# Kernel tuning notes

Measured on AMD Instinct MI355X. Metric: run time of the kernel, lower is better.

The kernel has to match this reference:

```python
import jax, jax.numpy as jnp
import numpy as np

B, D_W, D_C, D_P = 4096, 2048, 1024, 2048
RANK = D_W // 4  # 512, per A_U/A_V shapes (d_w, d_w//4)


def setup_inputs() -> dict:
    key = jax.random.key(0)
    ks = jax.random.split(key, 10)
    return {
        "w_prev": jax.random.normal(ks[0], (B, D_W), jnp.float32),
        "z_t": jax.random.normal(ks[1], (B, D_P), jnp.float32),
        "c_t": jax.random.normal(ks[2], (B, D_C), jnp.float32),
        # params (mirroring flax init: A_diag zeros, A_U/A_V normal(0.01),
        # Dense kernels lecun_normal-ish scale, zero biases)
        "A_diag": jnp.zeros((D_W,), jnp.float32),
        "A_U": 0.01 * jax.random.normal(ks[3], (D_W, RANK), jnp.float32),
        "A_V": 0.01 * jax.random.normal(ks[4], (D_W, RANK), jnp.float32),
        "W_mod": jax.random.normal(ks[5], (D_C, D_W), jnp.float32) / np.sqrt(D_C),
        "b_mod": jnp.zeros((D_W,), jnp.float32),
        "W_B": jax.random.normal(ks[6], (D_C + D_P, D_W), jnp.float32) / np.sqrt(D_C + D_P),
        "b_B": jnp.zeros((D_W,), jnp.float32),
    }


def reference(w_prev, z_t, c_t, A_diag, A_U, A_V, W_mod, b_mod, W_B, b_B):
    # A = diag(tanh(A_diag)*0.9) + A_U @ A_V^T, row-scaled by modulation.
    # Equivalent (same math) without materializing [B, d_w, d_w]:
    #   (A * m[:, :, None]) @ w = m * (a_diag * w + A_U @ (A_V^T @ w))
    a_diag = jnp.tanh(A_diag) * 0.9                              # [d_w]
    modulation = jnp.tanh(c_t @ W_mod + b_mod)                   # [B, d_w]
    Aw = a_diag * w_prev + (w_prev @ A_V) @ A_U.T                # [B, d_w]
    Bt = jnp.concatenate([c_t, z_t], axis=-1) @ W_B + b_B        # [B, d_w]
    return modulation * Aw + Bt
```

## Files before the change

kernel.cpp:

```cpp
#include <hip/hip_runtime.h>


#define DEV __device__ __forceinline__

typedef __bf16 v8bf __attribute__((ext_vector_type(8)));
typedef __bf16 v4bf __attribute__((ext_vector_type(4)));
typedef float  v4f  __attribute__((ext_vector_type(4)));

typedef __attribute__((address_space(1))) const unsigned int* as1_cuint_ptr;
typedef __attribute__((address_space(3))) unsigned int*       as3_uint_ptr;

DEV void async16(const void* g, void* l) {
  __builtin_amdgcn_global_load_lds(
      (as1_cuint_ptr)(unsigned long long)g,
      (as3_uint_ptr)(unsigned long long)l,
      16, 0, 0);
}

DEV float tanh_fast(float x) {
  x = fminf(15.f, fmaxf(-15.f, x));
  float e = __expf(2.f * x);
  return (e - 1.f) / (e + 1.f);
}

__global__ void prep(const float* __restrict__ w, const float* __restrict__ z,
                     const float* __restrict__ c, const float* __restrict__ au,
                     const float* __restrict__ av,
                     const float* __restrict__ Wmod, const float* __restrict__ WB,
                     __bf16* __restrict__ wb, __bf16* __restrict__ zb,
                     __bf16* __restrict__ cb, __bf16* __restrict__ aub,
                     __bf16* __restrict__ avb,
                     __bf16* __restrict__ Wmodt, __bf16* __restrict__ WBt) {
  __shared__ float t[32][33];
  int b = blockIdx.x;
  if (b < 22528) {
    const float* src; __bf16* dst; int off;
    if (b < 8192)        { src = w;  dst = wb;  off = b; }
    else if (b < 16384)  { src = z;  dst = zb;  off = b - 8192; }
    else if (b < 20480)  { src = c;  dst = cb;  off = b - 16384; }
    else if (b < 21504)  { src = au; dst = aub; off = b - 20480; }
    else                 { src = av; dst = avb; off = b - 21504; }
    size_t i = (size_t)off * 1024 + (size_t)threadIdx.x * 4;
    float4 v = *reinterpret_cast<const float4*>(src + i);
    v4bf o;
    o.x = (__bf16)v.x; o.y = (__bf16)v.y; o.z = (__bf16)v.z; o.w = (__bf16)v.w;
    *reinterpret_cast<v4bf*>(dst + i) = o;
    return;
  }
  b -= 22528;
  const float* src; __bf16* dst; int R;
  if (b < 2048) { src = Wmod; dst = Wmodt; R = 1024; }
  else          { b -= 2048; src = WB; dst = WBt; R = 3072; }
  const int c0 = (b & 63) * 32, r0 = (b >> 6) * 32;
  const int C = 2048;
  const int tx = threadIdx.x & 31, ty = threadIdx.x >> 5;
#pragma unroll
  for (int rr = 0; rr < 32; rr += 8)
    t[ty + rr][tx] = src[(size_t)(r0 + ty + rr) * C + c0 + tx];
  __syncthreads();
#pragma unroll
  for (int rr = 0; rr < 32; rr += 8)
    dst[(size_t)(c0 + ty + rr) * R + r0 + tx] = (__bf16)t[tx][ty + rr];
}

__global__ __launch_bounds__(256, 2) void gemm_mt(
    const __bf16* __restrict__ A0, const __bf16* __restrict__ Bt,
    int N, int K, __bf16* __restrict__ out, const float* __restrict__ A_diag) {
  __shared__ __align__(16) __bf16 As[128 * 32];
  __shared__ __align__(16) __bf16 Bs[128 * 32];

  const int tid = threadIdx.x, lane = tid & 63, wid = tid >> 6;
  const int wm = wid >> 1, wn = wid & 1, l16 = lane & 15, quad = lane >> 4;
  const int m0 = blockIdx.y * 128, n0 = blockIdx.x * 128;
  const int sg_row = lane >> 2;
  const int sk = ((lane & 3) ^ ((lane >> 3) & 3)) * 8;
  const int qs = quad ^ ((l16 >> 1) & 3);

  v4f acc[4][4];
#pragma unroll
  for (int i = 0; i < 4; ++i)
#pragma unroll
    for (int j = 0; j < 4; ++j) { v4f zz = {0,0,0,0}; acc[i][j] = zz; }

  for (int k0 = 0; k0 < K; k0 += 32) {
    __syncthreads();
#pragma unroll
    for (int t = 0; t < 2; ++t) {
      const int chunk = wid * 2 + t;
      const int row = chunk * 16 + sg_row;
      async16((const void*)(A0 + (size_t)(m0 + row) * K + k0 + sk),
              (void*)&As[chunk * 512 + lane * 8]);
      async16((const void*)(Bt + (size_t)(n0 + row) * K + k0 + sk),
              (void*)&Bs[chunk * 512 + lane * 8]);
    }
    __syncthreads();
    const v8bf* Ap = reinterpret_cast<const v8bf*>(As);
    const v8bf* Bp = reinterpret_cast<const v8bf*>(Bs);
    v8bf a[4], b[4];
#pragma unroll
    for (int i = 0; i < 4; ++i) a[i] = Ap[(wm * 64 + i * 16 + l16) * 4 + qs];
#pragma unroll
    for (int j = 0; j < 4; ++j) b[j] = Bp[(wn * 64 + j * 16 + l16) * 4 + qs];
#pragma unroll
    for (int i = 0; i < 4; ++i)
#pragma unroll
      for (int j = 0; j < 4; ++j)
        acc[i][j] = __builtin_amdgcn_mfma_f32_16x16x32_bf16(a[i], b[j],
                                                            acc[i][j], 0, 0, 0);
  }

  const int mBase = m0 + wm * 64 + quad * 4;
  const int nBase = n0 + wn * 64 + l16;
#pragma unroll
  for (int j = 0; j < 4; ++j) {
    const int n = nBase + j * 16;
#pragma unroll
    for (int i = 0; i < 4; ++i)
#pragma unroll
      for (int r = 0; r < 4; ++r) {
        const int m = mBase + i * 16 + r;
        float v = acc[i][j][r];
        if (m == n) v += tanh_fast(A_diag[m]) * 0.9f;
        out[(size_t)m * N + n] = (__bf16)v;
      }
  }
}

__global__ __launch_bounds__(256, 2) void fused_main(
    const __bf16* __restrict__ c, const __bf16* __restrict__ z,
    const __bf16* __restrict__ w, const __bf16* __restrict__ Wmodt,
    const __bf16* __restrict__ Mt, const __bf16* __restrict__ WBt,
    const float* __restrict__ b_mod, const float* __restrict__ b_B,
    float* __restrict__ out) {
  constexpr int DC = 1024, DW = 2048, KB = 3072;
  __shared__ __align__(16) __bf16 As[128 * 128];
  __shared__ __align__(16) __bf16 Bs[128 * 128];

  const int tid = threadIdx.x, lane = tid & 63, wid = tid >> 6;
  const int wm = wid >> 1, wn = wid & 1, l16 = lane & 15, quad = lane >> 4;
  const int m0 = blockIdx.y * 128;
  const int n0 = blockIdx.x * 128;
  const int r4  = lane >> 4;
  const int s16 = lane & 15;

  v4f acc[4][4];
#pragma unroll
  for (int i = 0; i < 4; ++i)
#pragma unroll
    for (int j = 0; j < 4; ++j) { v4f zz = {0,0,0,0}; acc[i][j] = zz; }

  auto kstep = [&](const __bf16* gA, size_t lda, const __bf16* gB, size_t ldb,
                   int kA, int kB) {
    __syncthreads();
#pragma unroll
    for (int t = 0; t < 8; ++t) {
      const int row = wid * 32 + t * 4 + r4;
      const int gk = (s16 ^ (row & 15)) * 8;
      async16((const void*)(gA + (size_t)(m0 + row) * lda + kA + gk),
              (void*)&As[row * 128 + s16 * 8]);
      async16((const void*)(gB + (size_t)(n0 + row) * ldb + kB + gk),
              (void*)&Bs[row * 128 + s16 * 8]);
    }
    __syncthreads();
    const v8bf* Ap = reinterpret_cast<const v8bf*>(As);
    const v8bf* Bp = reinterpret_cast<const v8bf*>(Bs);
#pragma unroll
    for (int s = 0; s < 4; ++s) {
      const int rs = (s * 4 + quad) ^ l16;
      v8bf a[4], b[4];
#pragma unroll
      for (int i = 0; i < 4; ++i)
        a[i] = Ap[(wm * 64 + i * 16 + l16) * 16 + rs];
#pragma unroll
      for (int j = 0; j < 4; ++j)
        b[j] = Bp[(wn * 64 + j * 16 + l16) * 16 + rs];
#pragma unroll
      for (int i = 0; i < 4; ++i)
#pragma unroll
        for (int j = 0; j < 4; ++j)
          acc[i][j] = __builtin_amdgcn_mfma_f32_16x16x32_bf16(
              a[i], b[j], acc[i][j], 0, 0, 0);
    }
  };

  const int nBase = n0 + wn * 64 + l16;

  for (int k0 = 0; k0 < DC; k0 += 128) kstep(c, DC, Wmodt, DC, k0, k0);

  v4f mod_s[4][4];
#pragma unroll
  for (int j = 0; j < 4; ++j) {
    const float bn = b_mod[nBase + j * 16];
#pragma unroll
    for (int i = 0; i < 4; ++i) {
#pragma unroll
      for (int r = 0; r < 4; ++r)
        mod_s[i][j][r] = tanh_fast(acc[i][j][r] + bn);
      v4f zz = {0,0,0,0};
      acc[i][j] = zz;
    }
  }

  for (int k0 = 0; k0 < DW; k0 += 128) kstep(w, DW, Mt, DW, k0, k0);

#pragma unroll
  for (int i = 0; i < 4; ++i)
#pragma unroll
    for (int j = 0; j < 4; ++j) acc[i][j] *= mod_s[i][j];

  for (int k0 = 0; k0 < DC; k0 += 128) kstep(c, DC, WBt, KB, k0, k0);
  for (int k0 = DC; k0 < KB; k0 += 128) kstep(z, DW, WBt, KB, k0 - DC, k0);

  const int mBase = m0 + wm * 64 + quad * 4;
#pragma unroll
  for (int j = 0; j < 4; ++j) {
    const int n = nBase + j * 16;
    const float bn = b_B[n];
#pragma unroll
    for (int i = 0; i < 4; ++i)
#pragma unroll
      for (int r = 0; r < 4; ++r) {
        const int m = mBase + i * 16 + r;
        out[(size_t)m * DW + n] = acc[i][j][r] + bn;
      }
  }
}


extern "C" void kernel_launch(void* const* d_in, const int* in_sizes, int n_in,
                              void* d_out, int out_size, void* d_ws,
                              size_t ws_size, hipStream_t stream) {
  const float* w_prev = (const float*)d_in[0];
  const float* z_t    = (const float*)d_in[1];
  const float* c_t    = (const float*)d_in[2];
  const float* A_diag = (const float*)d_in[3];
  const float* A_U    = (const float*)d_in[4];
  const float* A_V    = (const float*)d_in[5];
  const float* W_mod  = (const float*)d_in[6];
  const float* b_mod  = (const float*)d_in[7];
  const float* W_B    = (const float*)d_in[8];
  const float* b_B    = (const float*)d_in[9];

  constexpr int Bsz = 4096, DW = 2048, RK = 512;
  const size_t MB = 1ull << 20;
  char* ws = (char*)d_ws;
  __bf16* w_bf  = (__bf16*)(ws + 0);
  __bf16* z_bf  = (__bf16*)(ws + 16 * MB);
  __bf16* c_bf  = (__bf16*)(ws + 32 * MB);
  __bf16* AU_bf = (__bf16*)(ws + 40 * MB);
  __bf16* AV_bf = (__bf16*)(ws + 42 * MB);
  __bf16* Wmodt = (__bf16*)(ws + 44 * MB);
  __bf16* WBt   = (__bf16*)(ws + 48 * MB);
  __bf16* Mt    = (__bf16*)(ws + 60 * MB);

  prep<<<30720, 256, 0, stream>>>(w_prev, z_t, c_t, A_U, A_V, W_mod, W_B,
                                  w_bf, z_bf, c_bf, AU_bf, AV_bf, Wmodt, WBt);

  gemm_mt<<<dim3(DW / 128, DW / 128), 256, 0, stream>>>(AU_bf, AV_bf, DW, RK,
                                                        Mt, A_diag);

  fused_main<<<dim3(DW / 128, Bsz / 128), 256, 0, stream>>>(
      c_bf, z_bf, w_bf, Wmodt, Mt, WBt, b_mod, b_B, (float*)d_out);
}
```

Measured before the change: 282.5 us.

## Triple-buffer fused GEMM with async prefetch, 256x128 tiles, and block swizzle

After: 308.3 us. +9.1%, slower.

```diff
diff --git a/kernel.cpp b/kernel.cpp
--- a/kernel.cpp
+++ b/kernel.cpp
@@ -58,9 +58,14 @@
   for (int rr = 0; rr < 32; rr += 8)
     t[ty + rr][tx] = src[(size_t)(r0 + ty + rr) * C + c0 + tx];
   __syncthreads();
-#pragma unroll
-  for (int rr = 0; rr < 32; rr += 8)
-    dst[(size_t)(c0 + ty + rr) * R + r0 + tx] = (__bf16)t[tx][ty + rr];
+  const int orow = threadIdx.x >> 3;
+  const int oc   = (threadIdx.x & 7) * 4;
+  v4bf o;
+  o.x = (__bf16)t[oc + 0][orow];
+  o.y = (__bf16)t[oc + 1][orow];
+  o.z = (__bf16)t[oc + 2][orow];
+  o.w = (__bf16)t[oc + 3][orow];
+  *reinterpret_cast<v4bf*>(&dst[(size_t)(c0 + orow) * R + r0 + oc]) = o;
 }
 
 __global__ __launch_bounds__(256, 2) void gemm_mt(
@@ -126,103 +131,145 @@
   }
 }
 
-__global__ __launch_bounds__(256, 2) void fused_main(
+__global__ __launch_bounds__(512, 2) void fused_main(
     const __bf16* __restrict__ c, const __bf16* __restrict__ z,
     const __bf16* __restrict__ w, const __bf16* __restrict__ Wmodt,
     const __bf16* __restrict__ Mt, const __bf16* __restrict__ WBt,
     const float* __restrict__ b_mod, const float* __restrict__ b_B,
     float* __restrict__ out) {
-  constexpr int DC = 1024, DW = 2048, KB = 3072;
-  __shared__ __align__(16) __bf16 As[128 * 128];
-  __shared__ __align__(16) __bf16 Bs[128 * 128];
+  constexpr int DC = 1024, DW = 2048, KB3 = 3072;
+  constexpr int AT = 256 * 64;
+  constexpr int BT = 128 * 64;
+  constexpr int NT = 96;
+  __shared__ __align__(16) __bf16 As[3 * AT];
+  __shared__ __align__(16) __bf16 Bs[3 * BT];
 
   const int tid = threadIdx.x, lane = tid & 63, wid = tid >> 6;
-  const int wm = wid >> 1, wn = wid & 1, l16 = lane & 15, quad = lane >> 4;
-  const int m0 = blockIdx.y * 128;
-  const int n0 = blockIdx.x * 128;
-  const int r4  = lane >> 4;
-  const int s16 = lane & 15;
+  const int wm = wid >> 1, wn = wid & 1;
+  const int l16 = lane & 15, quad = lane >> 4, l8 = l16 & 7;
+  const int s8 = lane & 7, r8 = lane >> 3;
+
+  const int flat = blockIdx.y * 16 + blockIdx.x;
+  const int swz = (flat & 7) * 32 + (flat >> 3);
+  const int m0 = (swz >> 4) * 256;
+  const int n0 = (swz & 15) * 128;
+
+  const int nBase = n0 + wn * 64 + l16;
+  float bmodr[4], bBr[4];
+#pragma unroll
+  for (int j = 0; j < 4; ++j) {
+    bmodr[j] = b_mod[nBase + j * 16];
+    bBr[j]   = b_B[nBase + j * 16];
+  }
+
+  auto stage = [&](int T) {
+    const __bf16* gA; const __bf16* gB; int lda, ldb, kA, kB;
+    if (T < 16)      { gA = c; lda = DC; kA = T << 6;        gB = Wmodt; ldb = DC;  kB = T << 6; }
+    else if (T < 48) { gA = w; lda = DW; kA = (T - 16) << 6; gB = Mt;    ldb = DW;  kB = (T - 16) << 6; }
+    else if (T < 64) { gA = c; lda = DC; kA = (T - 48) << 6; gB = WBt;   ldb = KB3; kB = (T - 48) << 6; }
+    else             { gA = z; lda = DW; kA = (T - 64) << 6; gB = WBt;   ldb = KB3; kB = DC + ((T - 64) << 6); }
+    __bf16* Ab = &As[(T % 3) * AT];
+    __bf16* Bb = &Bs[(T % 3) * BT];
+#pragma unroll
+    for (int q = 0; q < 4; ++q) {
+      const int row = wid * 32 + q * 8 + r8;
+      const int gk = (s8 ^ (row & 7)) << 3;
+      async16((const void*)(gA + (size_t)(m0 + row) * lda + kA + gk),
+              (void*)&Ab[row * 64 + s8 * 8]);
+    }
+#pragma unroll
+    for (int q = 0; q < 2; ++q) {
+      const int row = wid * 16 + q * 8 + r8;
+      const int gk = (s8 ^ (row & 7)) << 3;
+      async16((const void*)(gB + (size_t)(n0 + row) * ldb + kB + gk),
+              (void*)&Bb[row * 64 + s8 * 8]);
+    }
+  };
 
   v4f acc[4][4];
 #pragma unroll
   for (int i = 0; i < 4; ++i)
 #pragma unroll
     for (int j = 0; j < 4; ++j) { v4f zz = {0,0,0,0}; acc[i][j] = zz; }
-
-  auto kstep = [&](const __bf16* gA, size_t lda, const __bf16* gB, size_t ldb,
-                   int kA, int kB) {
-    __syncthreads();
-#pragma unroll
-    for (int t = 0; t < 8; ++t) {
-      const int row = wid * 32 + t * 4 + r4;
-      const int gk = (s16 ^ (row & 15)) * 8;
-      async16((const void*)(gA + (size_t)(m0 + row) * lda + kA + gk),
-              (void*)&As[row * 128 + s16 * 8]);
-      async16((const void*)(gB + (size_t)(n0 + row) * ldb + kB + gk),
-              (void*)&Bs[row * 128 + s16 * 8]);
-    }
-    __syncthreads();
-    const v8bf* Ap = reinterpret_cast<const v8bf*>(As);
-    const v8bf* Bp = reinterpret_cast<const v8bf*>(Bs);
-#pragma unroll
-    for (int s = 0; s < 4; ++s) {
-      const int rs = (s * 4 + quad) ^ l16;
-      v8bf a[4], b[4];
+  v4bf mod_b[4][4];
+
+  stage(0); stage(1);
+  asm volatile("s_waitcnt vmcnt(6)" ::: "memory");
+  __builtin_amdgcn_s_barrier();
+  asm volatile("" ::: "memory");
+
+  for (int t = 0; t < NT; ++t) {
+    if (t + 2 < NT) stage(t + 2);
+
+    const v8bf* Ap = reinterpret_cast<const v8bf*>(&As[(t % 3) * AT]);
+    const v8bf* Bp = reinterpret_cast<const v8bf*>(&Bs[(t % 3) * BT]);
+
+    v8bf bfr[4][2];
+#pragma unroll
+    for (int j = 0; j < 4; ++j)
+#pragma unroll
+      for (int ks = 0; ks < 2; ++ks)
+        bfr[j][ks] = Bp[(wn * 64 + j * 16 + l16) * 8 + ((ks * 4 + quad) ^ l8)];
+
+#pragma unroll
+    for (int ih = 0; ih < 2; ++ih) {
+      v8bf afr[2][2];
+#pragma unroll
+      for (int ii = 0; ii < 2; ++ii)
+#pragma unroll
+        for (int ks = 0; ks < 2; ++ks)
+          afr[ii][ks] =
+              Ap[(wm * 64 + (ih * 2 + ii) * 16 + l16) * 8 + ((ks * 4 + quad) ^ l8)];
+      __builtin_amdgcn_s_setprio(1);
+#pragma unroll
+      for (int ii = 0; ii < 2; ++ii)
+#pragma unroll
+        for (int j = 0; j < 4; ++j)
+#pragma unroll
+          for (int ks = 0; ks < 2; ++ks)
+            acc[ih * 2 + ii][j] = __builtin_amdgcn_mfma_f32_16x16x32_bf16(
+                afr[ii][ks], bfr[j][ks], acc[ih * 2 + ii][j], 0, 0, 0);
+      __builtin_amdgcn_s_setprio(0);
+    }
+
+    if (t + 2 < NT) asm volatile("s_waitcnt vmcnt(6)" ::: "memory");
+    else            asm volatile("s_waitcnt vmcnt(0)" ::: "memory");
+    __builtin_amdgcn_s_barrier();
+    asm volatile("" ::: "memory");
+
+    if (t == 15) {
 #pragma unroll
       for (int i = 0; i < 4; ++i)
-        a[i] = Ap[(wm * 64 + i * 16 + l16) * 16 + rs];
-#pragma unroll
-      for (int j = 0; j < 4; ++j)
-        b[j] = Bp[(wn * 64 + j * 16 + l16) * 16 + rs];
+#pragma unroll
+        for (int j = 0; j < 4; ++j) {
+          v4bf mb;
+#pragma unroll
+          for (int r = 0; r < 4; ++r)
+            mb[r] = (__bf16)tanh_fast(acc[i][j][r] + bmodr[j]);
+          mod_b[i][j] = mb;
+          v4f zz = {0,0,0,0};
+          acc[i][j] = zz;
+        }
+    } else if (t == 47) {
 #pragma unroll
       for (int i = 0; i < 4; ++i)
 #pragma unroll
         for (int j = 0; j < 4; ++j)
-          acc[i][j] = __builtin_amdgcn_mfma_f32_16x16x32_bf16(
-              a[i], b[j], acc[i][j], 0, 0, 0);
-    }
-  };
-
-  const int nBase = n0 + wn * 64 + l16;
-
-  for (int k0 = 0; k0 < DC; k0 += 128) kstep(c, DC, Wmodt, DC, k0, k0);
-
-  v4f mod_s[4][4];
-#pragma unroll
-  for (int j = 0; j < 4; ++j) {
-    const float bn = b_mod[nBase + j * 16];
-#pragma unroll
-    for (int i = 0; i < 4; ++i) {
-#pragma unroll
-      for (int r = 0; r < 4; ++r)
-        mod_s[i][j][r] = tanh_fast(acc[i][j][r] + bn);
-      v4f zz = {0,0,0,0};
-      acc[i][j] = zz;
-    }
-  }
-
-  for (int k0 = 0; k0 < DW; k0 += 128) kstep(w, DW, Mt, DW, k0, k0);
-
-#pragma unroll
-  for (int i = 0; i < 4; ++i)
-#pragma unroll
-    for (int j = 0; j < 4; ++j) acc[i][j] *= mod_s[i][j];
-
-  for (int k0 = 0; k0 < DC; k0 += 128) kstep(c, DC, WBt, KB, k0, k0);
-  for (int k0 = DC; k0 < KB; k0 += 128) kstep(z, DW, WBt, KB, k0 - DC, k0);
+#pragma unroll
+          for (int r = 0; r < 4; ++r)
+            acc[i][j][r] *= (float)mod_b[i][j][r];
+    }
+  }
 
   const int mBase = m0 + wm * 64 + quad * 4;
 #pragma unroll
   for (int j = 0; j < 4; ++j) {
     const int n = nBase + j * 16;
-    const float bn = b_B[n];
 #pragma unroll
     for (int i = 0; i < 4; ++i)
 #pragma unroll
-      for (int r = 0; r < 4; ++r) {
-        const int m = mBase + i * 16 + r;
-        out[(size_t)m * DW + n] = acc[i][j][r] + bn;
-      }
+      for (int r = 0; r < 4; ++r)
+        out[(size_t)(mBase + i * 16 + r) * DW + n] = acc[i][j][r] + bBr[j];
   }
 }
 
@@ -259,6 +306,6 @@
   gemm_mt<<<dim3(DW / 128, DW / 128), 256, 0, stream>>>(AU_bf, AV_bf, DW, RK,
                                                         Mt, A_diag);
 
-  fused_main<<<dim3(DW / 128, Bsz / 128), 256, 0, stream>>>(
+  fused_main<<<dim3(16, 16), 512, 0, stream>>>(
       c_bf, z_bf, w_bf, Wmodt, Mt, WBt, b_mod, b_B, (float*)d_out);
 }
```

## Fuse low-rank M GEMM into prep kernel, converting A_U/A_V to bf16 on the fly

Applied to the files above, without the earlier changes.

New measurement: 285.3 us. About the same (+1.0%).

```diff
diff --git a/kernel.cpp b/kernel.cpp
--- a/kernel.cpp
+++ b/kernel.cpp
@@ -23,23 +23,96 @@
   return (e - 1.f) / (e + 1.f);
 }
 
-__global__ void prep(const float* __restrict__ w, const float* __restrict__ z,
-                     const float* __restrict__ c, const float* __restrict__ au,
-                     const float* __restrict__ av,
-                     const float* __restrict__ Wmod, const float* __restrict__ WB,
-                     __bf16* __restrict__ wb, __bf16* __restrict__ zb,
-                     __bf16* __restrict__ cb, __bf16* __restrict__ aub,
-                     __bf16* __restrict__ avb,
-                     __bf16* __restrict__ Wmodt, __bf16* __restrict__ WBt) {
-  __shared__ float t[32][33];
+__global__ __launch_bounds__(256, 2) void prep_gemm(
+    const float* __restrict__ w, const float* __restrict__ z,
+    const float* __restrict__ c, const float* __restrict__ au,
+    const float* __restrict__ av, const float* __restrict__ Wmod,
+    const float* __restrict__ WB, const float* __restrict__ A_diag,
+    __bf16* __restrict__ wb, __bf16* __restrict__ zb, __bf16* __restrict__ cb,
+    __bf16* __restrict__ Wmodt, __bf16* __restrict__ WBt,
+    __bf16* __restrict__ Mt) {
+  __shared__ __align__(16) char smem[16384];
   int b = blockIdx.x;
-  if (b < 22528) {
+
+  if (b < 256) {
+    __bf16* As = (__bf16*)smem;
+    __bf16* Bs = (__bf16*)(smem + 8192);
+    const int tid = threadIdx.x, lane = tid & 63, wid = tid >> 6;
+    const int wm = wid >> 1, wn = wid & 1, l16 = lane & 15, quad = lane >> 4;
+    const int m0 = (b >> 4) * 128, n0 = (b & 15) * 128;
+    const int qs = quad ^ ((l16 >> 1) & 3);
+    const int row = tid >> 1, sp = (tid & 1) * 2;
+
+    v4f acc[4][4];
+#pragma unroll
+    for (int i = 0; i < 4; ++i)
+#pragma unroll
+      for (int j = 0; j < 4; ++j) { v4f zz = {0, 0, 0, 0}; acc[i][j] = zz; }
+
+    for (int k0 = 0; k0 < 512; k0 += 32) {
+      __syncthreads();
+#pragma unroll
+      for (int ss = 0; ss < 2; ++ss) {
+        const int s = sp + ss;
+        const int gk = (s ^ ((row >> 1) & 3)) * 8;
+        const float* pa = au + (size_t)(m0 + row) * 512 + k0 + gk;
+        const float* pb = av + (size_t)(n0 + row) * 512 + k0 + gk;
+        float4 a0 = *reinterpret_cast<const float4*>(pa);
+        float4 a1 = *reinterpret_cast<const float4*>(pa + 4);
+        float4 b0 = *reinterpret_cast<const float4*>(pb);
+        float4 b1 = *reinterpret_cast<const float4*>(pb + 4);
+        v8bf va, vb;
+        va[0] = (__bf16)a0.x; va[1] = (__bf16)a0.y;
+        va[2] = (__bf16)a0.z; va[3] = (__bf16)a0.w;
+        va[4] = (__bf16)a1.x; va[5] = (__bf16)a1.y;
+        va[6] = (__bf16)a1.z; va[7] = (__bf16)a1.w;
+        vb[0] = (__bf16)b0.x; vb[1] = (__bf16)b0.y;
+        vb[2] = (__bf16)b0.z; vb[3] = (__bf16)b0.w;
+        vb[4] = (__bf16)b1.x; vb[5] = (__bf16)b1.y;
+        vb[6] = (__bf16)b1.z; vb[7] = (__bf16)b1.w;
+        *reinterpret_cast<v8bf*>(&As[row * 32 + s * 8]) = va;
+        *reinterpret_cast<v8bf*>(&Bs[row * 32 + s * 8]) = vb;
+      }
+      __syncthreads();
+      const v8bf* Ap = reinterpret_cast<const v8bf*>(As);
+      const v8bf* Bp = reinterpret_cast<const v8bf*>(Bs);
+      v8bf a[4], bb[4];
+#pragma unroll
+      for (int i = 0; i < 4; ++i) a[i] = Ap[(wm * 64 + i * 16 + l16) * 4 + qs];
+#pragma unroll
+      for (int j = 0; j < 4; ++j) bb[j] = Bp[(wn * 64 + j * 16 + l16) * 4 + qs];
+#pragma unroll
+      for (int i = 0; i < 4; ++i)
+#pragma unroll
+        for (int j = 0; j < 4; ++j)
+          acc[i][j] = __builtin_amdgcn_mfma_f32_16x16x32_bf16(a[i], bb[j],
+                                                              acc[i][j], 0, 0, 0);
+    }
+
+    const int mBase = m0 + wm * 64 + quad * 4;
+    const int nBase = n0 + wn * 64 + l16;
+#pragma unroll
+    for (int j = 0; j < 4; ++j) {
+      const int n = nBase + j * 16;
+#pragma unroll
+      for (int i = 0; i < 4; ++i)
+#pragma unroll
+        for (int r = 0; r < 4; ++r) {
+          const int m = mBase + i * 16 + r;
+          float v = acc[i][j][r];
+          if (m == n) v += tanh_fast(A_diag[m]) * 0.9f;
+          Mt[(size_t)m * 2048 + n] = (__bf16)v;
+        }
+    }
+    return;
+  }
+
+  b -= 256;
+  if (b < 20480) {
     const float* src; __bf16* dst; int off;
-    if (b < 8192)        { src = w;  dst = wb;  off = b; }
-    else if (b < 16384)  { src = z;  dst = zb;  off = b - 8192; }
-    else if (b < 20480)  { src = c;  dst = cb;  off = b - 16384; }
-    else if (b < 21504)  { src = au; dst = aub; off = b - 20480; }
-    else                 { src = av; dst = avb; off = b - 21504; }
+    if (b < 8192)       { src = w; dst = wb; off = b; }
+    else if (b < 16384) { src = z; dst = zb; off = b - 8192; }
+    else                { src = c; dst = cb; off = b - 16384; }
     size_t i = (size_t)off * 1024 + (size_t)threadIdx.x * 4;
     float4 v = *reinterpret_cast<const float4*>(src + i);
     v4bf o;
@@ -47,7 +120,9 @@
     *reinterpret_cast<v4bf*>(dst + i) = o;
     return;
   }
-  b -= 22528;
+
+  b -= 20480;
+  float (*t)[33] = (float(*)[33])smem;
   const float* src; __bf16* dst; int R;
   if (b < 2048) { src = Wmod; dst = Wmodt; R = 1024; }
   else          { b -= 2048; src = WB; dst = WBt; R = 3072; }
@@ -58,72 +133,14 @@
   for (int rr = 0; rr < 32; rr += 8)
     t[ty + rr][tx] = src[(size_t)(r0 + ty + rr) * C + c0 + tx];
   __syncthreads();
-#pragma unroll
-  for (int rr = 0; rr < 32; rr += 8)
-    dst[(size_t)(c0 + ty + rr) * R + r0 + tx] = (__bf16)t[tx][ty + rr];
-}
-
-__global__ __launch_bounds__(256, 2) void gemm_mt(
-    const __bf16* __restrict__ A0, const __bf16* __restrict__ Bt,
-    int N, int K, __bf16* __restrict__ out, const float* __restrict__ A_diag) {
-  __shared__ __align__(16) __bf16 As[128 * 32];
-  __shared__ __align__(16) __bf16 Bs[128 * 32];
-
-  const int tid = threadIdx.x, lane = tid & 63, wid = tid >> 6;
-  const int wm = wid >> 1, wn = wid & 1, l16 = lane & 15, quad = lane >> 4;
-  const int m0 = blockIdx.y * 128, n0 = blockIdx.x * 128;
-  const int sg_row = lane >> 2;
-  const int sk = ((lane & 3) ^ ((lane >> 3) & 3)) * 8;
-  const int qs = quad ^ ((l16 >> 1) & 3);
-
-  v4f acc[4][4];
-#pragma unroll
-  for (int i = 0; i < 4; ++i)
-#pragma unroll
-    for (int j = 0; j < 4; ++j) { v4f zz = {0,0,0,0}; acc[i][j] = zz; }
-
-  for (int k0 = 0; k0 < K; k0 += 32) {
-    __syncthreads();
-#pragma unroll
-    for (int t = 0; t < 2; ++t) {
-      const int chunk = wid * 2 + t;
-      const int row = chunk * 16 + sg_row;
-      async16((const void*)(A0 + (size_t)(m0 + row) * K + k0 + sk),
-              (void*)&As[chunk * 512 + lane * 8]);
-      async16((const void*)(Bt + (size_t)(n0 + row) * K + k0 + sk),
-              (void*)&Bs[chunk * 512 + lane * 8]);
-    }
-    __syncthreads();
-    const v8bf* Ap = reinterpret_cast<const v8bf*>(As);
-    const v8bf* Bp = reinterpret_cast<const v8bf*>(Bs);
-    v8bf a[4], b[4];
-#pragma unroll
-    for (int i = 0; i < 4; ++i) a[i] = Ap[(wm * 64 + i * 16 + l16) * 4 + qs];
-#pragma unroll
-    for (int j = 0; j < 4; ++j) b[j] = Bp[(wn * 64 + j * 16 + l16) * 4 + qs];
-#pragma unroll
-    for (int i = 0; i < 4; ++i)
-#pragma unroll
-      for (int j = 0; j < 4; ++j)
-        acc[i][j] = __builtin_amdgcn_mfma_f32_16x16x32_bf16(a[i], b[j],
-                                                            acc[i][j], 0, 0, 0);
-  }
-
-  const int mBase = m0 + wm * 64 + quad * 4;
-  const int nBase = n0 + wn * 64 + l16;
-#pragma unroll
-  for (int j = 0; j < 4; ++j) {
-    const int n = nBase + j * 16;
-#pragma unroll
-    for (int i = 0; i < 4; ++i)
-#pragma unroll
-      for (int r = 0; r < 4; ++r) {
-        const int m = mBase + i * 16 + r;
-        float v = acc[i][j][r];
-        if (m == n) v += tanh_fast(A_diag[m]) * 0.9f;
-        out[(size_t)m * N + n] = (__bf16)v;
-      }
-  }
+  const int orow = threadIdx.x >> 3;
+  const int oc   = (threadIdx.x & 7) * 4;
+  v4bf o;
+  o.x = (__bf16)t[oc + 0][orow];
+  o.y = (__bf16)t[oc + 1][orow];
+  o.z = (__bf16)t[oc + 2][orow];
+  o.w = (__bf16)t[oc + 3][orow];
+  *reinterpret_cast<v4bf*>(&dst[(size_t)(c0 + orow) * R + r0 + oc]) = o;
 }
 
 __global__ __launch_bounds__(256, 2) void fused_main(
@@ -241,23 +258,19 @@
   const float* W_B    = (const float*)d_in[8];
   const float* b_B    = (const float*)d_in[9];
 
-  constexpr int Bsz = 4096, DW = 2048, RK = 512;
+  constexpr int Bsz = 4096, DW = 2048;
   const size_t MB = 1ull << 20;
   char* ws = (char*)d_ws;
   __bf16* w_bf  = (__bf16*)(ws + 0);
   __bf16* z_bf  = (__bf16*)(ws + 16 * MB);
   __bf16* c_bf  = (__bf16*)(ws + 32 * MB);
-  __bf16* AU_bf = (__bf16*)(ws + 40 * MB);
-  __bf16* AV_bf = (__bf16*)(ws + 42 * MB);
-  __bf16* Wmodt = (__bf16*)(ws + 44 * MB);
-  __bf16* WBt   = (__bf16*)(ws + 48 * MB);
-  __bf16* Mt    = (__bf16*)(ws + 60 * MB);
-
-  prep<<<30720, 256, 0, stream>>>(w_prev, z_t, c_t, A_U, A_V, W_mod, W_B,
-                                  w_bf, z_bf, c_bf, AU_bf, AV_bf, Wmodt, WBt);
-
-  gemm_mt<<<dim3(DW / 128, DW / 128), 256, 0, stream>>>(AU_bf, AV_bf, DW, RK,
-                                                        Mt, A_diag);
+  __bf16* Wmodt = (__bf16*)(ws + 40 * MB);
+  __bf16* WBt   = (__bf16*)(ws + 44 * MB);
+  __bf16* Mt    = (__bf16*)(ws + 56 * MB);
+
+  prep_gemm<<<28928, 256, 0, stream>>>(w_prev, z_t, c_t, A_U, A_V, W_mod, W_B,
+                                       A_diag, w_bf, z_bf, c_bf, Wmodt, WBt,
+                                       Mt);
 
   fused_main<<<dim3(DW / 128, Bsz / 128), 256, 0, stream>>>(
       c_bf, z_bf, w_bf, Wmodt, Mt, WBt, b_mod, b_B, (float*)d_out);
```
